# Kernel tuning notes

Hardware: AMD Instinct MI355X
Metric: run time of the kernel (lower is better)

The kernel has to match this reference:

```python
import jax, jax.numpy as jnp
import numpy as np

EPS = 1e-8
SIGMA_MIN = 1e-4
B, T, C, P = 32, 8192, 64, 168


def setup_inputs() -> dict:
    key = jax.random.key(0)
    k1, k2, k3, k4, k5 = jax.random.split(key, 5)
    x_full = jax.random.normal(k1, (B, T, C), dtype=jnp.float32)
    mask = (jax.random.uniform(k2, (B, T, C)) > 0.2).astype(jnp.float32)
    x = mask * x_full  # observed input with missing positions zeroed
    phase_id = jax.random.randint(k3, (B,), 0, P, dtype=jnp.int64)
    anchor_mu = jax.random.normal(k4, (P, C), dtype=jnp.float32)
    anchor_log_sigma = 0.1 * jax.random.normal(k5, (P, C), dtype=jnp.float32)
    return {
        "x": x,
        "mask": mask,
        "phase_id": phase_id,
        "anchor_mu": anchor_mu,
        "anchor_log_sigma": anchor_log_sigma,
        "tau0_raw": jnp.zeros((1,), dtype=jnp.float32),
        "tau1_raw": jnp.zeros((1,), dtype=jnp.float32),
        "missing_token": jnp.zeros((1, 1, C), dtype=jnp.float32),
    }


def _max_gap_ratio(mask):
    # longest contiguous missing run (channel 0) as fraction of T -> (B,1,1)
    missing = mask[:, :, 0] < 0.5  # (B, T)
    Tlen = missing.shape[1]
    idx = jnp.arange(Tlen)[None, :]  # (1, T)
    # index of most recent observed position (running max), -1 if none yet
    last_obs = jax.lax.associative_scan(jnp.maximum,
                                        jnp.where(missing, -1, idx), axis=1)
    run = jnp.where(missing, idx - last_obs, 0)  # current missing run length
    max_run = run.max(axis=1).astype(jnp.float32)
    return (max_run / Tlen)[:, None, None]


def reference(x, mask, phase_id, anchor_mu, anchor_log_sigma,
              tau0_raw, tau1_raw, missing_token):
    # masked moments over time axis
    mask_sum = jnp.clip(mask.sum(axis=1, keepdims=True), EPS, None)  # (B,1,C)
    mu_obs = (mask * x).sum(axis=1, keepdims=True) / mask_sum
    var_obs = (mask * (x - mu_obs) ** 2).sum(axis=1, keepdims=True) / mask_sum
    sigma_obs = jnp.sqrt(var_obs + EPS)

    # anchor lookup
    mu_ref = anchor_mu[phase_id][:, None, :]              # (B,1,C)
    log_sigma_ref = anchor_log_sigma[phase_id][:, None, :]

    coverage = mask.mean(axis=1, keepdims=True)           # (B,1,C)
    gap_ratio = _max_gap_ratio(mask)                      # (B,1,1)

    tau0 = jax.nn.softplus(tau0_raw)
    tau1 = jax.nn.softplus(tau1_raw)
    w = coverage / (coverage + tau0 + tau1 * gap_ratio + EPS)

    mu = w * mu_obs + (1.0 - w) * mu_ref
    log_sigma = w * jnp.log(sigma_obs + EPS) + (1.0 - w) * log_sigma_ref
    sigma = jnp.clip(jnp.exp(log_sigma), SIGMA_MIN, None)

    z = (x - mu) / sigma
    return mask * z + (1.0 - mask) * missing_token
```

## Files before the change

### kernel.cpp

```cpp
#include <hip/hip_runtime.h>
#include <math.h>

#define B_ 32
#define T_ 8192
#define C_ 64
#define S_ 128
#define L_ (T_ / S_)
#define EPS_ 1e-8f
#define SIGMA_MIN_ 1e-4f

#define SUM_OFF 0
#define SQ_OFF  262144
#define MS_OFF  524288
#define GAP_OFF 786432
#define MU_OFF  802816
#define INV_OFF 804864

__device__ inline float4 f4add(float4 a, float4 b) {
    return make_float4(a.x + b.x, a.y + b.y, a.z + b.z, a.w + b.w);
}
__device__ inline float4 f4shfl_xor(float4 v, int m) {
    float4 r;
    r.x = __shfl_xor(v.x, m);
    r.y = __shfl_xor(v.y, m);
    r.z = __shfl_xor(v.z, m);
    r.w = __shfl_xor(v.w, m);
    return r;
}

__global__ __launch_bounds__(256) void k1_stats(const float* __restrict__ x,
                                                const float* __restrict__ mask,
                                                float* __restrict__ ws) {
    const int bid = blockIdx.x;
    const int b   = bid >> 7;
    const int s   = bid & (S_ - 1);
    const int tid = threadIdx.x;
    const int cq  = tid & 15;
    const int row = (tid >> 4) & 3;
    const int wv  = tid >> 6;

    const float4* x4 = (const float4*)x;
    const float4* m4 = (const float4*)mask;
    const long base = ((long)b * T_ + (long)s * L_) * 16 + cq;

    float4 xv[4], mv[4];
#pragma unroll
    for (int it = 0; it < 4; ++it) {
        long idx = base + (long)(it * 16 + wv * 4 + row) * 16;
        xv[it] = x4[idx];
        mv[it] = m4[idx];
    }

    float4 s1 = make_float4(0.f, 0.f, 0.f, 0.f);
    float4 s2 = make_float4(0.f, 0.f, 0.f, 0.f);
    float4 sm = make_float4(0.f, 0.f, 0.f, 0.f);
#pragma unroll
    for (int it = 0; it < 4; ++it) {
        s1.x += xv[it].x; s1.y += xv[it].y; s1.z += xv[it].z; s1.w += xv[it].w;
        s2.x += xv[it].x * xv[it].x; s2.y += xv[it].y * xv[it].y;
        s2.z += xv[it].z * xv[it].z; s2.w += xv[it].w * xv[it].w;
        sm.x += mv[it].x; sm.y += mv[it].y; sm.z += mv[it].z; sm.w += mv[it].w;
    }

    s1 = f4add(s1, f4shfl_xor(s1, 16)); s1 = f4add(s1, f4shfl_xor(s1, 32));
    s2 = f4add(s2, f4shfl_xor(s2, 16)); s2 = f4add(s2, f4shfl_xor(s2, 32));
    sm = f4add(sm, f4shfl_xor(sm, 16)); sm = f4add(sm, f4shfl_xor(sm, 32));

    __shared__ float4 shA[4][16];
    __shared__ float4 shB[4][16];
    __shared__ float4 shC[4][16];
    if ((tid & 63) < 16) { shA[wv][cq] = s1; shB[wv][cq] = s2; shC[wv][cq] = sm; }
    __syncthreads();

    if (tid < 16) {
        float4 a = f4add(f4add(shA[0][tid], shA[1][tid]), f4add(shA[2][tid], shA[3][tid]));
        float4 c = f4add(f4add(shB[0][tid], shB[1][tid]), f4add(shB[2][tid], shB[3][tid]));
        float4 e = f4add(f4add(shC[0][tid], shC[1][tid]), f4add(shC[2][tid], shC[3][tid]));
        const int o = (bid * C_ + tid * 4) >> 2;
        ((float4*)(ws + SUM_OFF))[o] = a;
        ((float4*)(ws + SQ_OFF ))[o] = c;
        ((float4*)(ws + MS_OFF ))[o] = e;
    }

    if (tid < 64) {
        const float m0 = mask[((long)b * T_ + (long)s * L_ + tid) * C_];
        unsigned long long bal = __ballot(m0 < 0.5f);
        if (tid == 0) {
            int pre, suf, best;
            if (bal == ~0ull) {
                pre = 64; suf = 64; best = 64;
            } else {
                pre = __builtin_ctzll(~bal);
                suf = __builtin_clzll(~bal);
                unsigned long long tmp = bal; best = 0;
                while (tmp) { tmp &= (tmp << 1); ++best; }
            }
            int* gp = (int*)(ws + GAP_OFF) + bid * 4;
            gp[0] = pre; gp[1] = suf; gp[2] = best;
        }
    }
}

__global__ __launch_bounds__(256) void k2_params(const int*   __restrict__ phase_id,
                                                 const float* __restrict__ anchor_mu,
                                                 const float* __restrict__ anchor_ls,
                                                 const float* __restrict__ tau0_raw,
                                                 const float* __restrict__ tau1_raw,
                                                 float* __restrict__ ws) {
    const int b   = blockIdx.x;
    const int tid = threadIdx.x;
    const int c   = tid & 63;
    const int p   = tid >> 6;

    __shared__ float sh_gap;
    __shared__ float sh[3][4][64];

    if (tid == 0) {
        const int* gp = (const int*)(ws + GAP_OFF) + b * S_ * 4;
        int pre = 0, suf = 0, best = 0, len = 0;
        for (int s = 0; s < S_; ++s) {
            int p_i = gp[s * 4], s_i = gp[s * 4 + 1], b_i = gp[s * 4 + 2];
            if (s == 0) { pre = p_i; suf = s_i; best = b_i; len = L_; }
            else {
                int cross = suf + p_i;
                best = max(best, max(b_i, cross));
                pre  = (pre == len) ? len + p_i : pre;
                suf  = (s_i == L_) ? suf + L_ : s_i;
                len += L_;
            }
        }
        sh_gap = (float)best / (float)T_;
    }

    float sum = 0.f, sq = 0.f, ms = 0.f;
    for (int s = p; s < S_; s += 4) {
        int o = (b * S_ + s) * C_ + c;
        sum += ws[SUM_OFF + o];
        sq  += ws[SQ_OFF  + o];
        ms  += ws[MS_OFF  + o];
    }
    sh[0][p][c] = sum; sh[1][p][c] = sq; sh[2][p][c] = ms;
    __syncthreads();

    if (tid < 64) {
        sum = sh[0][0][c] + sh[0][1][c] + sh[0][2][c] + sh[0][3][c];
        sq  = sh[1][0][c] + sh[1][1][c] + sh[1][2][c] + sh[1][3][c];
        ms  = sh[2][0][c] + sh[2][1][c] + sh[2][2][c] + sh[2][3][c];

        const float msc    = fmaxf(ms, EPS_);
        const float mu_obs = sum / msc;
        float var = (sq - 2.f * mu_obs * sum + mu_obs * mu_obs * ms) / msc;
        var = fmaxf(var, 0.f);
        const float sigma_obs = sqrtf(var + EPS_);
        const float coverage  = ms / (float)T_;

        const float t0 = log1pf(expf(tau0_raw[0]));
        const float t1 = log1pf(expf(tau1_raw[0]));
        const float w  = coverage / (coverage + t0 + t1 * sh_gap + EPS_);

        const int   pid    = phase_id[b];
        const float mu_ref = anchor_mu[pid * C_ + c];
        const float ls_ref = anchor_ls[pid * C_ + c];

        const float mu = w * mu_obs + (1.f - w) * mu_ref;
        const float ls = w * logf(sigma_obs + EPS_) + (1.f - w) * ls_ref;
        const float sigma = fmaxf(expf(ls), SIGMA_MIN_);

        ws[MU_OFF  + b * C_ + c] = mu;
        ws[INV_OFF + b * C_ + c] = 1.f / sigma;
    }
}

__global__ __launch_bounds__(256) void k3_norm(const float* __restrict__ x,
                                               const float* __restrict__ mask,
                                               const float* __restrict__ token,
                                               const float* __restrict__ ws,
                                               float* __restrict__ out) {
    const int gid = blockIdx.x * 256 + threadIdx.x;
    const float4* x4 = (const float4*)x;
    const float4* m4 = (const float4*)mask;
    const float4* mu4  = (const float4*)(ws + MU_OFF);
    const float4* inv4 = (const float4*)(ws + INV_OFF);
    const float4* tk4  = (const float4*)token;

    const int b = gid >> 17;
    const int p = b * 16 + (gid & 15);

    float4 xv = x4[gid];
    float4 mv = m4[gid];
    float4 mu = mu4[p];
    float4 iv = inv4[p];
    float4 tk = tk4[gid & 15];

    float4 o;
    o.x = mv.x * ((xv.x - mu.x) * iv.x) + (1.f - mv.x) * tk.x;
    o.y = mv.y * ((xv.y - mu.y) * iv.y) + (1.f - mv.y) * tk.y;
    o.z = mv.z * ((xv.z - mu.z) * iv.z) + (1.f - mv.z) * tk.z;
    o.w = mv.w * ((xv.w - mu.w) * iv.w) + (1.f - mv.w) * tk.w;

    ((float4*)out)[gid] = o;
}

extern "C" void kernel_launch(void* const* d_in, const int* in_sizes, int n_in,
                              void* d_out, int out_size, void* d_ws, size_t ws_size,
                              hipStream_t stream) {
    const float* x    = (const float*)d_in[0];
    const float* mask = (const float*)d_in[1];
    const int*   pid  = (const int*)  d_in[2];
    const float* amu  = (const float*)d_in[3];
    const float* als  = (const float*)d_in[4];
    const float* t0   = (const float*)d_in[5];
    const float* t1   = (const float*)d_in[6];
    const float* tok  = (const float*)d_in[7];
    float* out = (float*)d_out;
    float* ws  = (float*)d_ws;

    k1_stats<<<B_ * S_, 256, 0, stream>>>(x, mask, ws);
    k2_params<<<B_, 256, 0, stream>>>(pid, amu, als, t0, t1, ws);
    const int n4 = B_ * T_ * C_ / 4;
    k3_norm<<<n4 / 256, 256, 0, stream>>>(x, mask, tok, ws, out);
}
```

Measured before the change: 75.20 us.

## Halve stats blocks, derive gap bits from loaded mask, parallelize gap merge

Cuts the number of first-pass blocks per batch from 128 to 64, so each thread loads 8 rows instead of 4, with all loads issued before the accumulation. The missing-run bits now come from the already-loaded mask through a shared byte array rather than a separate strided global read. The serial 128-step gap merge in the parameter kernel becomes a 64-lane butterfly reduction over (prefix, suffix, best, length) tuples. The cost is fewer blocks in flight and more registers per thread in the stats kernel.

```diff
diff --git a/kernel.cpp b/kernel.cpp
--- a/kernel.cpp
+++ b/kernel.cpp
@@ -4,17 +4,17 @@
 #define B_ 32
 #define T_ 8192
 #define C_ 64
-#define S_ 128
+#define S_ 64
 #define L_ (T_ / S_)
 #define EPS_ 1e-8f
 #define SIGMA_MIN_ 1e-4f
 
 #define SUM_OFF 0
-#define SQ_OFF  262144
-#define MS_OFF  524288
-#define GAP_OFF 786432
-#define MU_OFF  802816
-#define INV_OFF 804864
+#define SQ_OFF  131072
+#define MS_OFF  262144
+#define GAP_OFF 393216
+#define MU_OFF  401408
+#define INV_OFF 403456
 
 __device__ inline float4 f4add(float4 a, float4 b) {
     return make_float4(a.x + b.x, a.y + b.y, a.z + b.z, a.w + b.w);
@@ -28,47 +28,62 @@
     return r;
 }
 
+__device__ inline void word_tuple(unsigned long long w, int& pre, int& suf, int& best) {
+    if (w == ~0ull) { pre = 64; suf = 64; best = 64; return; }
+    pre = __builtin_ctzll(~w);
+    suf = __builtin_clzll(~w);
+    unsigned long long tmp = w; best = 0;
+    while (tmp) { tmp &= (tmp << 1); ++best; }
+}
+
 __global__ __launch_bounds__(256) void k1_stats(const float* __restrict__ x,
                                                 const float* __restrict__ mask,
                                                 float* __restrict__ ws) {
     const int bid = blockIdx.x;
-    const int b   = bid >> 7;
+    const int b   = bid >> 6;
     const int s   = bid & (S_ - 1);
     const int tid = threadIdx.x;
     const int cq  = tid & 15;
-    const int row = (tid >> 4) & 3;
+    const int tr  = tid >> 4;
     const int wv  = tid >> 6;
 
     const float4* x4 = (const float4*)x;
     const float4* m4 = (const float4*)mask;
-    const long base = ((long)b * T_ + (long)s * L_) * 16 + cq;
-
-    float4 xv[4], mv[4];
-#pragma unroll
-    for (int it = 0; it < 4; ++it) {
-        long idx = base + (long)(it * 16 + wv * 4 + row) * 16;
-        xv[it] = x4[idx];
-        mv[it] = m4[idx];
-    }
+    const long base = ((long)b * T_ + (long)s * L_ + tr) * 16 + cq;
+
+    float4 xa[8], ma[8];
+#pragma unroll
+    for (int it = 0; it < 8; ++it) xa[it] = x4[base + (long)(it * 16) * 16];
+#pragma unroll
+    for (int it = 0; it < 8; ++it) ma[it] = m4[base + (long)(it * 16) * 16];
+    __builtin_amdgcn_sched_barrier(0);
 
     float4 s1 = make_float4(0.f, 0.f, 0.f, 0.f);
     float4 s2 = make_float4(0.f, 0.f, 0.f, 0.f);
     float4 sm = make_float4(0.f, 0.f, 0.f, 0.f);
 #pragma unroll
-    for (int it = 0; it < 4; ++it) {
-        s1.x += xv[it].x; s1.y += xv[it].y; s1.z += xv[it].z; s1.w += xv[it].w;
-        s2.x += xv[it].x * xv[it].x; s2.y += xv[it].y * xv[it].y;
-        s2.z += xv[it].z * xv[it].z; s2.w += xv[it].w * xv[it].w;
-        sm.x += mv[it].x; sm.y += mv[it].y; sm.z += mv[it].z; sm.w += mv[it].w;
+    for (int it = 0; it < 8; ++it) {
+        s1.x += xa[it].x; s1.y += xa[it].y; s1.z += xa[it].z; s1.w += xa[it].w;
+        s2.x += xa[it].x * xa[it].x; s2.y += xa[it].y * xa[it].y;
+        s2.z += xa[it].z * xa[it].z; s2.w += xa[it].w * xa[it].w;
+        sm.x += ma[it].x; sm.y += ma[it].y; sm.z += ma[it].z; sm.w += ma[it].w;
+    }
+
+    __shared__ float4 shA[4][16];
+    __shared__ float4 shB[4][16];
+    __shared__ float4 shC[4][16];
+    __shared__ unsigned char misbyte[L_];
+
+    if (cq == 0) {
+#pragma unroll
+        for (int it = 0; it < 8; ++it)
+            misbyte[it * 16 + tr] = (ma[it].x < 0.5f) ? 1 : 0;
     }
 
     s1 = f4add(s1, f4shfl_xor(s1, 16)); s1 = f4add(s1, f4shfl_xor(s1, 32));
     s2 = f4add(s2, f4shfl_xor(s2, 16)); s2 = f4add(s2, f4shfl_xor(s2, 32));
     sm = f4add(sm, f4shfl_xor(sm, 16)); sm = f4add(sm, f4shfl_xor(sm, 32));
 
-    __shared__ float4 shA[4][16];
-    __shared__ float4 shB[4][16];
-    __shared__ float4 shC[4][16];
     if ((tid & 63) < 16) { shA[wv][cq] = s1; shB[wv][cq] = s2; shC[wv][cq] = sm; }
     __syncthreads();
 
@@ -83,20 +98,18 @@
     }
 
     if (tid < 64) {
-        const float m0 = mask[((long)b * T_ + (long)s * L_ + tid) * C_];
-        unsigned long long bal = __ballot(m0 < 0.5f);
+        const int m0 = misbyte[tid];
+        const int m1 = misbyte[64 + tid];
+        unsigned long long w0 = __ballot(m0 != 0);
+        unsigned long long w1 = __ballot(m1 != 0);
         if (tid == 0) {
-            int pre, suf, best;
-            if (bal == ~0ull) {
-                pre = 64; suf = 64; best = 64;
-            } else {
-                pre = __builtin_ctzll(~bal);
-                suf = __builtin_clzll(~bal);
-                unsigned long long tmp = bal; best = 0;
-                while (tmp) { tmp &= (tmp << 1); ++best; }
-            }
-            int* gp = (int*)(ws + GAP_OFF) + bid * 4;
-            gp[0] = pre; gp[1] = suf; gp[2] = best;
+            int p0, s0, b0, p1, s1i, b1;
+            word_tuple(w0, p0, s0, b0);
+            word_tuple(w1, p1, s1i, b1);
+            int pre  = (p0 == 64) ? 64 + p1 : p0;
+            int suf  = (s1i == 64) ? s0 + 64 : s1i;
+            int best = max(max(b0, b1), s0 + p1);
+            ((int4*)((int*)(ws + GAP_OFF)))[bid] = make_int4(pre, suf, best, L_);
         }
     }
 }
@@ -115,21 +128,29 @@
     __shared__ float sh_gap;
     __shared__ float sh[3][4][64];
 
-    if (tid == 0) {
-        const int* gp = (const int*)(ws + GAP_OFF) + b * S_ * 4;
-        int pre = 0, suf = 0, best = 0, len = 0;
-        for (int s = 0; s < S_; ++s) {
-            int p_i = gp[s * 4], s_i = gp[s * 4 + 1], b_i = gp[s * 4 + 2];
-            if (s == 0) { pre = p_i; suf = s_i; best = b_i; len = L_; }
-            else {
-                int cross = suf + p_i;
-                best = max(best, max(b_i, cross));
-                pre  = (pre == len) ? len + p_i : pre;
-                suf  = (s_i == L_) ? suf + L_ : s_i;
-                len += L_;
+    if (tid < 64) {
+        int4 t4 = ((const int4*)((const int*)(ws + GAP_OFF)))[b * S_ + tid];
+        int pre = t4.x, suf = t4.y, best = t4.z, len = t4.w;
+#pragma unroll
+        for (int m = 1; m < 64; m <<= 1) {
+            int ppre = __shfl_xor(pre, m);
+            int psuf = __shfl_xor(suf, m);
+            int pbest = __shfl_xor(best, m);
+            int plen = __shfl_xor(len, m);
+            int l_pre, l_suf, l_best, l_len, r_pre, r_suf, r_best, r_len;
+            if (tid & m) {
+                l_pre = ppre; l_suf = psuf; l_best = pbest; l_len = plen;
+                r_pre = pre;  r_suf = suf;  r_best = best;  r_len = len;
+            } else {
+                l_pre = pre;  l_suf = suf;  l_best = best;  l_len = len;
+                r_pre = ppre; r_suf = psuf; r_best = pbest; r_len = plen;
             }
+            best = max(max(l_best, r_best), l_suf + r_pre);
+            pre  = (l_pre == l_len) ? l_len + r_pre : l_pre;
+            suf  = (r_suf == r_len) ? r_len + l_suf : r_suf;
+            len  = l_len + r_len;
         }
-        sh_gap = (float)best / (float)T_;
+        if (tid == 0) sh_gap = (float)best / (float)T_;
     }
 
     float sum = 0.f, sq = 0.f, ms = 0.f;
```

After: 62.54 us. 16.8% less time.
